# Optimization experiments

Hardware: AMD Instinct MI355X
Metric: run time of the kernel (lower is better)

Reference implementation:

```python
import jax, jax.numpy as jnp
import numpy as np

# DeformConv hyperparameters (from init_kwargs)
KH, KW = 3, 3
STRIDE, PAD, DIL = 1, 1, 1
GROUPS, DG = 1, 1  # groups=1, deformable_groups=1
B, C, H, W = 4, 64, 128, 128
O = 64
HO = (H + 2 * PAD - (DIL * (KH - 1) + 1)) // STRIDE + 1  # 128
WO = (W + 2 * PAD - (DIL * (KW - 1) + 1)) // STRIDE + 1  # 128


def setup_inputs() -> dict:
    key = jax.random.key(0)
    k1, k2, k3, k4 = jax.random.split(key, 4)
    x = jax.random.normal(k1, (B, C, H, W), dtype=jnp.float32)
    # offset channels: dg * K * 2, ordered (y, x) per kernel tap (DCNv1 CUDA layout)
    offset = jax.random.normal(k2, (B, 2 * DG * KH * KW, HO, WO), dtype=jnp.float32)
    fan_in = C * KH * KW
    weight = jax.random.normal(k3, (O, C // GROUPS, KH, KW), dtype=jnp.float32) / np.sqrt(fan_in)
    bias = jax.random.normal(k4, (O,), dtype=jnp.float32) * 0.01
    return {"x": x, "offset": offset, "weight": weight, "bias": bias}


def _deform_sample(x, offset):
    """Bilinear-sample x at deformed kernel tap locations.
    Returns [B, C, K, HO, WO] where K = KH*KW."""
    K = KH * KW
    Cg = C // DG
    # offset -> [B, DG, K, 2, HO, WO]; channel layout: dg*2*K, pairs (y, x)
    off = offset.reshape(B, DG, K, 2, HO, WO)
    off_y, off_x = off[:, :, :, 0], off[:, :, :, 1]  # [B, DG, K, HO, WO]

    ki = (jnp.arange(K) // KW).astype(jnp.float32)  # kernel row
    kj = (jnp.arange(K) % KW).astype(jnp.float32)   # kernel col
    base_h = (jnp.arange(HO) * STRIDE - PAD).astype(jnp.float32)
    base_w = (jnp.arange(WO) * STRIDE - PAD).astype(jnp.float32)

    # sampling positions [B, DG, K, HO, WO]
    py = off_y + (ki * DIL)[None, None, :, None, None] + base_h[None, None, None, :, None]
    px = off_x + (kj * DIL)[None, None, :, None, None] + base_w[None, None, None, None, :]

    y0f = jnp.floor(py)
    x0f = jnp.floor(px)
    ly = py - y0f
    lx = px - x0f
    hy = 1.0 - ly
    hx = 1.0 - lx
    y0 = y0f.astype(jnp.int32)
    x0 = x0f.astype(jnp.int32)
    y1 = y0 + 1
    x1 = x0 + 1

    flat = x.reshape(B, DG, Cg, H * W)

    def gather(yi, xi, wgt):
        valid = (yi >= 0) & (yi < H) & (xi >= 0) & (xi < W)
        idx = jnp.clip(yi, 0, H - 1) * W + jnp.clip(xi, 0, W - 1)
        idx = idx.reshape(B, DG, 1, K * HO * WO)
        v = jnp.take_along_axis(flat, idx, axis=-1).reshape(B, DG, Cg, K, HO, WO)
        return v * (wgt * valid.astype(wgt.dtype))[:, :, None]

    val = (gather(y0, x0, hy * hx) + gather(y0, x1, hy * lx)
           + gather(y1, x0, ly * hx) + gather(y1, x1, ly * lx))
    return val.reshape(B, C, K, HO, WO)


def reference(x, offset, weight, bias):
    sampled = _deform_sample(x, offset)              # [B, C, K, HO, WO]
    w = weight.reshape(O, C, KH * KW)                # groups = 1
    out = jnp.einsum('bckhw,ock->bohw', sampled, w)  # im2col + GEMM
    return out + bias[None, :, None, None]
```

## Files before the change

kernel.cpp:

```cpp
#include <hip/hip_runtime.h>
#include <hip/hip_fp16.h>


#define B_  4
#define C_  64
#define H_  128
#define W_  128
#define O_  64
#define HO_ 128
#define WO_ 128
#define NCHUNK 8
#define NGW 12
#define NT_ 32
#define NROW 2
#define TR  16
#define TC  48
#define TSLOTS (TR * TC)
#define TBUF (TSLOTS * 8)
#define HW_ (H_ * W_)

typedef _Float16 half8 __attribute__((ext_vector_type(8)));
typedef __attribute__((ext_vector_type(4))) float f32x4;

union H8 { float4 v; __half2 h2[4]; half8 v8; };

__global__ __launch_bounds__(256)
void prep(const float* __restrict__ x, const float* __restrict__ w,
          __half* __restrict__ xt, __half* __restrict__ wt) {
    const int tid = threadIdx.x;
    if (blockIdx.x < 2048) {
        int t = blockIdx.x * 256 + tid;
        int xc = t & 127;
        int y  = (t >> 7) & 127;
        int ch = (t >> 14) & 7;
        int b  = t >> 17;
        const float* xp = x + (((size_t)(b * C_ + ch * 8) * H_) + y) * W_ + xc;
        union { __half h[8]; float4 v; } pk;
#pragma unroll
        for (int e = 0; e < 8; ++e) pk.h[e] = __float2half_rn(xp[e * H_ * W_]);
        *(float4*)(xt + (size_t)t * 8) = pk.v;
    } else {
        int t = (blockIdx.x - 2048) * 256 + tid;
        if (t >= NCHUNK * NGW * O_) return;
        int o  = t & 63;
        int g  = (t >> 6) % NGW;
        int ch = (t >> 6) / NGW;
        union { __half h[8]; float4 v; } pk;
#pragma unroll
        for (int e = 0; e < 8; ++e)
            pk.h[e] = (g < 9) ? __float2half_rn(w[(o * C_ + ch * 8 + e) * 9 + g])
                              : __half(0.0f);
        *(float4*)(wt + (size_t)t * 8) = pk.v;
    }
}

__global__ __launch_bounds__(256, 4)
void dcn_mfma(const __half* __restrict__ xt, const float* __restrict__ off,
              const __half* __restrict__ wt, const float* __restrict__ bias,
              float* __restrict__ out) {
    __shared__ __align__(16) _Float16 sT[2 * TBUF];

    const int tid = threadIdx.x;
    const int bid = blockIdx.x;
    const int w4  = bid & 3;
    const int hp  = (bid >> 2) & 63;
    const int b   = bid >> 8;
    const int ho  = hp << 1;
    const int woB = w4 * NT_;
    const int yb  = ho - 6;
    const int xb  = woB - 8;

    const int lane = tid & 63;
    const int wv   = tid >> 6;
    const int quad = lane >> 4;
    const int l15  = lane & 15;
    const int n    = wv * 16 + l15;
    const int hr   = ho + (n >> 5);
    const int wo   = woB + (n & 31);

    int a0_[3], a1_[3], nf_[3];
    __half2 ua2_[3], ub2_[3], va2_[3], vb2_[3];
#pragma unroll
    for (int ks = 0; ks < 3; ++ks) {
        int g = ks * 4 + quad;
        if (g < 9) {
            int ki = g / 3, kj = g - 3 * ki;
            float oy = off[(((b * 18) + 2 * g    ) * HO_ + hr) * WO_ + wo];
            float ox = off[(((b * 18) + 2 * g + 1) * HO_ + hr) * WO_ + wo];
            float py = (float)(hr - 1 + ki) + oy;
            float px = (float)(wo - 1 + kj) + ox;
            float y0f = floorf(py), x0f = floorf(px);
            int   y0 = (int)y0f,   x0 = (int)x0f;
            float ly = py - y0f,   lx = px - x0f;
            float hy = 1.f - ly,   hx = 1.f - lx;
            int y1 = y0 + 1, x1 = x0 + 1;
            float vy0 = (y0 >= 0 && y0 < H_) ? 1.f : 0.f;
            float vy1 = (y1 >= 0 && y1 < H_) ? 1.f : 0.f;
            float vx0 = (x0 >= 0 && x0 < W_) ? 1.f : 0.f;
            float vx1 = (x1 >= 0 && x1 < W_) ? 1.f : 0.f;
            int cy0 = min(max(y0, 0), H_ - 1), cy1 = min(max(y1, 0), H_ - 1);
            int ax  = min(max(x0, 0), W_ - 2);
            int cx0 = min(max(x0, 0), W_ - 1), cx1 = min(max(x1, 0), W_ - 1);
            float w00 = hy * hx * vy0 * vx0;
            float w01 = hy * lx * vy0 * vx1;
            float w10 = ly * hx * vy1 * vx0;
            float w11 = ly * lx * vy1 * vx1;
            float s0 = (cx0 != ax) ? 1.f : 0.f;
            float s1 = (cx1 != ax) ? 1.f : 0.f;
            int t0 = cy0 - yb, t1 = cy1 - yb, txx = ax - xb;
            int fb = ((unsigned)t0  > (TR - 1)) |
                     ((unsigned)t1  > (TR - 1)) |
                     ((unsigned)txx > (TC - 2));
            nf_[ks] = !fb;
            a0_[ks] = fb ? (cy0 * W_ + ax) : (t0 * TC + txx);
            a1_[ks] = fb ? (cy1 * W_ + ax) : (t1 * TC + txx);
            ua2_[ks] = __float2half2_rn(w00 * (1.f - s0) + w01 * (1.f - s1));
            ub2_[ks] = __float2half2_rn(w00 * s0 + w01 * s1);
            va2_[ks] = __float2half2_rn(w10 * (1.f - s0) + w11 * (1.f - s1));
            vb2_[ks] = __float2half2_rn(w10 * s0 + w11 * s1);
        } else {
            nf_[ks] = 1; a0_[ks] = 0; a1_[ks] = 0;
            ua2_[ks] = ub2_[ks] = va2_[ks] = vb2_[ks] = __float2half2_rn(0.f);
        }
    }

    int gofs[3];
#pragma unroll
    for (int j = 0; j < 3; ++j) {
        int s  = tid + j * 256;
        int rr = s / TC, cc = s - rr * TC;
        int yc = min(max(yb + rr, 0), H_ - 1);
        int xc = min(max(xb + cc, 0), W_ - 1);
        gofs[j] = yc * W_ + xc;
    }

    float4 pf0, pf1, pf2;
    auto issue = [&](int ch) {
        const float4* xc = (const float4*)(xt + ((size_t)(b * NCHUNK + ch)) * (HW_ * 8));
        pf0 = xc[gofs[0]];
        pf1 = xc[gofs[1]];
        pf2 = xc[gofs[2]];
    };
    auto tile_write = [&](int parity) {
        float4* tw = (float4*)(sT + parity * TBUF);
        tw[tid]       = pf0;
        tw[tid + 256] = pf1;
        tw[tid + 512] = pf2;
    };

    f32x4 acc[4];
#pragma unroll
    for (int ot = 0; ot < 4; ++ot) acc[ot] = (f32x4){0.f, 0.f, 0.f, 0.f};

    auto compute = [&](int ch) {
        const float4* tl  = (const float4*)(sT + (ch & 1) * TBUF);
        const float4* xcg = (const float4*)(xt + ((size_t)(b * NCHUNK + ch)) * (HW_ * 8));
        const __half* wc  = wt + (size_t)(ch * NGW) * O_ * 8;
#pragma unroll
        for (int ks = 0; ks < 3; ++ks) {
            int g = ks * 4 + quad;
            H8 q00, q01, q10, q11;
            if (nf_[ks]) {
                int a0 = a0_[ks], a1 = a1_[ks];
                q00.v = tl[a0];  q01.v = tl[a0 + 1];
                q10.v = tl[a1];  q11.v = tl[a1 + 1];
            } else {
                int a0 = a0_[ks], a1 = a1_[ks];
                q00.v = xcg[a0]; q01.v = xcg[a0 + 1];
                q10.v = xcg[a1]; q11.v = xcg[a1 + 1];
            }
            H8 s;
#pragma unroll
            for (int j = 0; j < 4; ++j) {
                __half2 t0 = __hmul2(ua2_[ks], q00.h2[j]);
                t0 = __hfma2(ub2_[ks], q01.h2[j], t0);
                t0 = __hfma2(va2_[ks], q10.h2[j], t0);
                t0 = __hfma2(vb2_[ks], q11.h2[j], t0);
                s.h2[j] = t0;
            }
#pragma unroll
            for (int ot = 0; ot < 4; ++ot) {
                half8 afr = *(const half8*)(wc + (size_t)(g * O_ + ot * 16 + l15) * 8);
                acc[ot] = __builtin_amdgcn_mfma_f32_16x16x32_f16(afr, s.v8, acc[ot], 0, 0, 0);
            }
        }
    };

    issue(0);
    tile_write(0);
    for (int ch = 0; ch < NCHUNK; ++ch) {
        __syncthreads();
        if (ch + 1 < NCHUNK) issue(ch + 1);
        compute(ch);
        if (ch + 1 < NCHUNK) tile_write((ch + 1) & 1);
    }

    {
        int row = wv >> 1;
        int woo = woB + (wv & 1) * 16 + l15;
        size_t base = (((size_t)(b * O_)) * HO_ + ho + row) * WO_ + woo;
#pragma unroll
        for (int ot = 0; ot < 4; ++ot)
#pragma unroll
            for (int rg = 0; rg < 4; ++rg) {
                int o = ot * 16 + quad * 4 + rg;
                out[base + (size_t)o * HO_ * WO_] = acc[ot][rg] + bias[o];
            }
    }
}

extern "C" void kernel_launch(void* const* d_in, const int* in_sizes, int n_in,
                              void* d_out, int out_size, void* d_ws, size_t ws_size,
                              hipStream_t stream) {
    const float* x    = (const float*)d_in[0];
    const float* off  = (const float*)d_in[1];
    const float* w    = (const float*)d_in[2];
    const float* bias = (const float*)d_in[3];
    float* out = (float*)d_out;

    __half* wt = (__half*)d_ws;
    __half* xt = (__half*)((char*)d_ws + 262144);

    hipLaunchKernelGGL(prep, dim3(2048 + 24), dim3(256), 0, stream, x, w, xt, wt);
    hipLaunchKernelGGL(dcn_mfma, dim3(B_ * (HO_ / NROW) * (WO_ / NT_)), dim3(256), 0, stream,
                       xt, off, wt, bias, out);
}
```

Measured before the change: 98.42 us.

## Stage input tiles via direct global-to-LDS loads and swizzle blocks across XCDs

Replaces the register round-trip (global load into float4 registers, then store to shared memory) with `__builtin_amdgcn_global_load_lds` 16-byte async copies straight into the double-buffered LDS tile. The prefetch is now issued before compute, with a single barrier after it. It also remaps blockIdx so that each XCD processes a contiguous range of tiles, improving L2 reuse of overlapping halo rows. This frees registers and removes the VGPR staging. It relies on the barrier waiting for the LDS-DMA loads to complete, and needs gfx950 support for the 16-byte variant.

```diff
diff --git a/kernel.cpp b/kernel.cpp
--- a/kernel.cpp
+++ b/kernel.cpp
@@ -61,7 +61,7 @@
     __shared__ __align__(16) _Float16 sT[2 * TBUF];
 
     const int tid = threadIdx.x;
-    const int bid = blockIdx.x;
+    const int bid = (blockIdx.x & 7) * 128 + (blockIdx.x >> 3);
     const int w4  = bid & 3;
     const int hp  = (bid >> 2) & 63;
     const int b   = bid >> 8;
@@ -134,18 +134,15 @@
         gofs[j] = yc * W_ + xc;
     }
 
-    float4 pf0, pf1, pf2;
-    auto issue = [&](int ch) {
-        const float4* xc = (const float4*)(xt + ((size_t)(b * NCHUNK + ch)) * (HW_ * 8));
-        pf0 = xc[gofs[0]];
-        pf1 = xc[gofs[1]];
-        pf2 = xc[gofs[2]];
-    };
-    auto tile_write = [&](int parity) {
-        float4* tw = (float4*)(sT + parity * TBUF);
-        tw[tid]       = pf0;
-        tw[tid + 256] = pf1;
-        tw[tid + 512] = pf2;
+    auto stage = [&](int ch, int parity) {
+        const char* xc = (const char*)(xt + ((size_t)(b * NCHUNK + ch)) * (HW_ * 8));
+        char* lb = (char*)sT + (size_t)parity * (TBUF * 2) + (size_t)(tid & ~63) * 16;
+#pragma unroll
+        for (int j = 0; j < 3; ++j)
+            __builtin_amdgcn_global_load_lds(
+                (const __attribute__((address_space(1))) unsigned int*)(xc + (size_t)gofs[j] * 16),
+                (__attribute__((address_space(3))) unsigned int*)(lb + j * 4096),
+                16, 0, 0);
     };
 
     f32x4 acc[4];
@@ -186,13 +183,12 @@
         }
     };
 
-    issue(0);
-    tile_write(0);
+    stage(0, 0);
+    __syncthreads();
     for (int ch = 0; ch < NCHUNK; ++ch) {
+        if (ch + 1 < NCHUNK) stage(ch + 1, (ch + 1) & 1);
+        compute(ch);
         __syncthreads();
-        if (ch + 1 < NCHUNK) issue(ch + 1);
-        compute(ch);
-        if (ch + 1 < NCHUNK) tile_write((ch + 1) & 1);
     }
 
     {
```

Result: no change. 96.60 us (-1.9%).
